# Kernel tuning notes

Hardware: AMD Instinct MI355X
Metric: run time of the kernel (lower is better)

The kernel has to match this reference:

```python
import jax, jax.numpy as jnp
import numpy as np

N_NODES = 50000


def gcn_conv(x, edge_index, W, b, n):
    # PyG GCNConv: xW, add self-loops, symmetric degree normalization,
    # scatter-add messages from source (row) to target (col).
    xw = x @ W
    row, col = edge_index[0], edge_index[1]
    loops = jnp.arange(n, dtype=edge_index.dtype)
    row = jnp.concatenate([row, loops])
    col = jnp.concatenate([col, loops])
    deg = jax.ops.segment_sum(jnp.ones(row.shape[0], dtype=xw.dtype), col, num_segments=n)
    dinv = jnp.where(deg > 0, jax.lax.rsqrt(deg), 0.0)
    norm = dinv[row] * dinv[col]  # [E+N]
    out = jax.ops.segment_sum(xw[row] * norm[:, None], col, num_segments=n)
    return out + b


def setup_inputs() -> dict:
    key = jax.random.key(0)
    ks = jax.random.split(key, 5)
    n, d_in, d_h, d_out, n_edges = N_NODES, 128, 128, 4, 600000
    x = jax.random.normal(ks[0], (n, d_in), dtype=jnp.float32)
    edge_index = jax.random.randint(ks[1], (2, n_edges), 0, n, dtype=jnp.int64)
    W1 = jax.random.normal(ks[2], (d_in, d_h), dtype=jnp.float32) * (1.0 / np.sqrt(d_in))
    b1 = jnp.zeros((d_h,), dtype=jnp.float32)
    W2 = jax.random.normal(ks[3], (d_h, d_h), dtype=jnp.float32) * (1.0 / np.sqrt(d_h))
    b2 = jnp.zeros((d_h,), dtype=jnp.float32)
    Wfc = jax.random.normal(ks[4], (2 * d_h, d_out), dtype=jnp.float32) * (1.0 / np.sqrt(2 * d_h))
    bfc = jnp.zeros((d_out,), dtype=jnp.float32)
    return {"x": x, "edge_index": edge_index, "W1": W1, "b1": b1,
            "W2": W2, "b2": b2, "Wfc": Wfc, "bfc": bfc}


def reference(x, edge_index, W1, b1, W2, b2, Wfc, bfc):
    n = x.shape[0]
    # dropout is identity at inference (training=False)
    h = jax.nn.relu(gcn_conv(x, edge_index, W1, b1, n))
    h = jax.nn.relu(gcn_conv(h, edge_index, W2, b2, n))
    # edge-level gather + concat + linear classifier
    edge_x = jnp.concatenate([h[edge_index[0]], h[edge_index[1]]], axis=-1)  # [E, 2*d_h]
    edge_scores = edge_x @ Wfc + bfc  # [E, d_out]
    return jax.nn.log_softmax(edge_scores, axis=1)
```

## Files before the change

kernel.cpp:

```cpp
#include <hip/hip_runtime.h>
#include <math.h>
#include <stdint.h>

#define D 128
#define SCAN_CHUNK 2048
#define LDA 136

typedef __attribute__((ext_vector_type(8))) short v8s;
typedef __attribute__((ext_vector_type(4))) float v4f;

static __device__ __forceinline__ uint16_t f2bf(float f) {
    uint32_t u = __float_as_uint(f);
    u = (u + 0x7fff + ((u >> 16) & 1)) >> 16;
    return (uint16_t)u;
}
static __device__ __forceinline__ float bf2f(uint16_t h) { return __uint_as_float((uint32_t)h << 16); }
static __device__ __forceinline__ float bf_lo(uint32_t u) { return __uint_as_float(u << 16); }
static __device__ __forceinline__ float bf_hi(uint32_t u) { return __uint_as_float(u & 0xffff0000u); }


__global__ void countpack_kernel(const int* __restrict__ col, int* __restrict__ cnt,
                                 int* __restrict__ rnk, int E,
                                 const float* __restrict__ W1, const float* __restrict__ W2,
                                 uint16_t* __restrict__ Wh, uint16_t* __restrict__ Wl) {
    int tid = blockIdx.x * blockDim.x + threadIdx.x;
    if (tid < 2 * 16384) {
        int layer = tid >> 14;
        int li = tid & 16383;
        int j = li & 7, lane = (li >> 3) & 63, f = li >> 9;
        int kstep = f >> 3, tile = f & 7;
        int k = kstep * 32 + ((lane >> 4) * 8) + j;
        int nn = tile * 16 + (lane & 15);
        const float* W = layer ? W2 : W1;
        float v = W[k * 128 + nn];
        uint16_t h = f2bf(v);
        Wh[tid] = h;
        Wl[tid] = f2bf(v - bf2f(h));
    }
    if (tid < E) rnk[tid] = atomicAdd(&cnt[col[tid]], 1);
}


__global__ __launch_bounds__(256) void scanA_kernel(const int* __restrict__ cnt,
                                                    int* __restrict__ bsum,
                                                    float* __restrict__ dinv, int n) {
    __shared__ int wsum[4];
    int b = blockIdx.x, t = threadIdx.x;
    int base = b * SCAN_CHUNK;
    int s = 0;
#pragma unroll
    for (int k = 0; k < SCAN_CHUNK / 256; k++) {
        int i = base + k * 256 + t;
        if (i < n) {
            int c = cnt[i];
            s += c;
            dinv[i] = rsqrtf((float)c + 1.0f);
        }
    }
#pragma unroll
    for (int off = 32; off > 0; off >>= 1) s += __shfl_xor(s, off, 64);
    if ((t & 63) == 0) wsum[t >> 6] = s;
    __syncthreads();
    if (t == 0) bsum[b] = wsum[0] + wsum[1] + wsum[2] + wsum[3];
}


__global__ __launch_bounds__(256) void scanC_kernel(const int* __restrict__ cnt,
                                                    const int* __restrict__ bsum,
                                                    int* __restrict__ offs, int n, int nb) {
    __shared__ int stage[SCAN_CHUNK];
    __shared__ int res[SCAN_CHUNK];
    __shared__ int tsum[256];
    __shared__ int sb[64];
    int b = blockIdx.x, t = threadIdx.x;
    if (t < 64) {
        int v = (t < nb) ? bsum[t] : 0;
        int inc = v;
#pragma unroll
        for (int off = 1; off < 64; off <<= 1) {
            int u = __shfl_up(inc, off, 64);
            if (t >= off) inc += u;
        }
        sb[t] = inc;
    }
    int base = b * SCAN_CHUNK;
#pragma unroll
    for (int k = 0; k < SCAN_CHUNK / 256; k++) {
        int i = base + k * 256 + t;
        stage[k * 256 + t] = (i < n) ? cnt[i] : 0;
    }
    __syncthreads();
    int my = 0;
#pragma unroll
    for (int j = 0; j < 8; j++) my += stage[t * 8 + j];
    tsum[t] = my;
    __syncthreads();
    for (int off = 1; off < 256; off <<= 1) {
        int v = (t >= off) ? tsum[t - off] : 0;
        __syncthreads();
        tsum[t] += v;
        __syncthreads();
    }
    int bbase = (b == 0) ? 0 : sb[b - 1];
    int run = tsum[t] - my + bbase;
#pragma unroll
    for (int j = 0; j < 8; j++) {
        res[t * 8 + j] = run;
        run += stage[t * 8 + j];
    }
    __syncthreads();
#pragma unroll
    for (int k = 0; k < SCAN_CHUNK / 256; k++) {
        int i = base + k * 256 + t;
        if (i < n) offs[i] = res[k * 256 + t];
    }
    if (b == gridDim.x - 1 && t == 0) offs[n] = sb[nb - 1];
}


static __device__ __forceinline__ void gemm_body(const uint16_t Ah[][LDA],
                                                 const uint16_t Al[][LDA],
                                                 const uint16_t* __restrict__ Wph,
                                                 const uint16_t* __restrict__ Wpl,
                                                 const float* __restrict__ dinv,
                                                 uint16_t* __restrict__ Cb,
                                                 int base_row, int M, int t) {
    int lane = t & 63, w = t >> 6;
    int m_l = lane & 15, quad = lane >> 4;
    int arow = w * 16 + m_l;

    v4f acc[8];
#pragma unroll
    for (int i = 0; i < 8; i++) acc[i] = (v4f){0.f, 0.f, 0.f, 0.f};

#pragma unroll
    for (int ks = 0; ks < 4; ks++) {
        v8s ah = *(const v8s*)&Ah[arow][ks * 32 + quad * 8];
        v8s al = *(const v8s*)&Al[arow][ks * 32 + quad * 8];
#pragma unroll
        for (int ti = 0; ti < 8; ti++) {
            int f = ks * 8 + ti;
            v8s bh = *(const v8s*)(Wph + ((size_t)(f * 64 + lane)) * 8);
            v8s bl = *(const v8s*)(Wpl + ((size_t)(f * 64 + lane)) * 8);
            acc[ti] = __builtin_amdgcn_mfma_f32_16x16x32_bf16(al, bh, acc[ti], 0, 0, 0);
            acc[ti] = __builtin_amdgcn_mfma_f32_16x16x32_bf16(ah, bl, acc[ti], 0, 0, 0);
            acc[ti] = __builtin_amdgcn_mfma_f32_16x16x32_bf16(ah, bh, acc[ti], 0, 0, 0);
        }
    }

    int rbase = base_row + w * 16 + quad * 4;
#pragma unroll
    for (int reg = 0; reg < 4; reg++) {
        int gr = rbase + reg;
        if (gr < M) {
            float di = dinv[gr];
#pragma unroll
            for (int ti = 0; ti < 8; ti++) {
                Cb[(size_t)gr * D + ti * 16 + m_l] = f2bf(di * acc[ti][reg]);
            }
        }
    }
}


__global__ __launch_bounds__(256) void fillgemm_kernel(const int* __restrict__ row,
                                                       const int* __restrict__ col,
                                                       const int* __restrict__ rnk,
                                                       const int* __restrict__ offs,
                                                       int* __restrict__ adj, int E,
                                                       const float* __restrict__ A,
                                                       const uint16_t* __restrict__ Wph,
                                                       const uint16_t* __restrict__ Wpl,
                                                       const float* __restrict__ dinv,
                                                       uint16_t* __restrict__ Cb, int M,
                                                       int nbG) {
    __shared__ uint16_t Ah[64][LDA];
    __shared__ uint16_t Al[64][LDA];
    int t = threadIdx.x;

    if (blockIdx.x >= nbG) {
        int e = (blockIdx.x - nbG) * 256 + t;
        if (e < E) adj[offs[col[e]] + rnk[e]] = row[e];
        return;
    }

    int base_row = blockIdx.x * 64;
#pragma unroll
    for (int kk = 0; kk < 8; kk++) {
        int idx = kk * 256 + t;
        int r = idx >> 5;
        int c4 = idx & 31;
        int gr = base_row + r;
        float4 f = (gr < M) ? *(const float4*)(A + (size_t)gr * D + c4 * 4)
                            : make_float4(0.f, 0.f, 0.f, 0.f);
        uint16_t h0 = f2bf(f.x), h1 = f2bf(f.y), h2 = f2bf(f.z), h3 = f2bf(f.w);
        uint16_t l0 = f2bf(f.x - bf2f(h0)), l1 = f2bf(f.y - bf2f(h1));
        uint16_t l2 = f2bf(f.z - bf2f(h2)), l3 = f2bf(f.w - bf2f(h3));
        *(ushort4*)&Ah[r][c4 * 4] = make_ushort4(h0, h1, h2, h3);
        *(ushort4*)&Al[r][c4 * 4] = make_ushort4(l0, l1, l2, l3);
    }
    __syncthreads();
    gemm_body(Ah, Al, Wph, Wpl, dinv, Cb, base_row, M, t);
}


__global__ __launch_bounds__(256) void agggemm_kernel(const uint32_t* __restrict__ xwb,
                                                      const int* __restrict__ adj,
                                                      const int* __restrict__ offs,
                                                      const float* __restrict__ dinv,
                                                      const float* __restrict__ bias,
                                                      const uint16_t* __restrict__ Wph,
                                                      const uint16_t* __restrict__ Wpl,
                                                      uint16_t* __restrict__ Cb, int M) {
    __shared__ uint16_t Ah[64][LDA];
    __shared__ uint16_t Al[64][LDA];
    int t = threadIdx.x, lane = t & 63, w = t >> 6;
    int base_row = blockIdx.x * 64;
    float2 bv = ((const float2*)bias)[lane];

    for (int rr = 0; rr < 8; rr++) {
        int rA = w * 16 + rr, rB = rA + 8;
        int iA = base_row + rA, iB = base_row + rB;
        float a0 = 0.f, a1 = 0.f, c0 = 0.f, c1 = 0.f;
        int jA = 0, eA = 0, jB = 0, eB = 0;
        if (iA < M) {
            uint32_t su = xwb[(size_t)iA * (D / 2) + lane];
            a0 = bf_lo(su); a1 = bf_hi(su);
            jA = offs[iA]; eA = offs[iA + 1];
        }
        if (iB < M) {
            uint32_t su = xwb[(size_t)iB * (D / 2) + lane];
            c0 = bf_lo(su); c1 = bf_hi(su);
            jB = offs[iB]; eB = offs[iB + 1];
        }
        while (jA + 7 < eA && jB + 7 < eB) {
            int xx[8], yy[8];
#pragma unroll
            for (int q = 0; q < 8; q++) { xx[q] = adj[jA + q]; yy[q] = adj[jB + q]; }
            uint32_t uA[8], uB[8];
#pragma unroll
            for (int q = 0; q < 8; q++) {
                uA[q] = xwb[(size_t)xx[q] * (D / 2) + lane];
                uB[q] = xwb[(size_t)yy[q] * (D / 2) + lane];
            }
#pragma unroll
            for (int q = 0; q < 8; q++) {
                a0 += bf_lo(uA[q]); a1 += bf_hi(uA[q]);
                c0 += bf_lo(uB[q]); c1 += bf_hi(uB[q]);
            }
            jA += 8; jB += 8;
        }
        for (; jA + 7 < eA; jA += 8) {
            int xx[8]; uint32_t uA[8];
#pragma unroll
            for (int q = 0; q < 8; q++) xx[q] = adj[jA + q];
#pragma unroll
            for (int q = 0; q < 8; q++) uA[q] = xwb[(size_t)xx[q] * (D / 2) + lane];
#pragma unroll
            for (int q = 0; q < 8; q++) { a0 += bf_lo(uA[q]); a1 += bf_hi(uA[q]); }
        }
        for (; jA + 3 < eA; jA += 4) {
            int x0 = adj[jA], x1 = adj[jA + 1], x2 = adj[jA + 2], x3 = adj[jA + 3];
            uint32_t u0 = xwb[(size_t)x0 * (D / 2) + lane];
            uint32_t u1 = xwb[(size_t)x1 * (D / 2) + lane];
            uint32_t u2 = xwb[(size_t)x2 * (D / 2) + lane];
            uint32_t u3 = xwb[(size_t)x3 * (D / 2) + lane];
            a0 += bf_lo(u0); a1 += bf_hi(u0);
            a0 += bf_lo(u1); a1 += bf_hi(u1);
            a0 += bf_lo(u2); a1 += bf_hi(u2);
            a0 += bf_lo(u3); a1 += bf_hi(u3);
        }
        for (; jA < eA; jA++) {
            uint32_t u = xwb[(size_t)adj[jA] * (D / 2) + lane];
            a0 += bf_lo(u); a1 += bf_hi(u);
        }
        for (; jB + 7 < eB; jB += 8) {
            int yy[8]; uint32_t uB[8];
#pragma unroll
            for (int q = 0; q < 8; q++) yy[q] = adj[jB + q];
#pragma unroll
            for (int q = 0; q < 8; q++) uB[q] = xwb[(size_t)yy[q] * (D / 2) + lane];
#pragma unroll
            for (int q = 0; q < 8; q++) { c0 += bf_lo(uB[q]); c1 += bf_hi(uB[q]); }
        }
        for (; jB + 3 < eB; jB += 4) {
            int y0 = adj[jB], y1 = adj[jB + 1], y2 = adj[jB + 2], y3 = adj[jB + 3];
            uint32_t u0 = xwb[(size_t)y0 * (D / 2) + lane];
            uint32_t u1 = xwb[(size_t)y1 * (D / 2) + lane];
            uint32_t u2 = xwb[(size_t)y2 * (D / 2) + lane];
            uint32_t u3 = xwb[(size_t)y3 * (D / 2) + lane];
            c0 += bf_lo(u0); c1 += bf_hi(u0);
            c0 += bf_lo(u1); c1 += bf_hi(u1);
            c0 += bf_lo(u2); c1 += bf_hi(u2);
            c0 += bf_lo(u3); c1 += bf_hi(u3);
        }
        for (; jB < eB; jB++) {
            uint32_t u = xwb[(size_t)adj[jB] * (D / 2) + lane];
            c0 += bf_lo(u); c1 += bf_hi(u);
        }
        float diA = (iA < M) ? dinv[iA] : 0.f;
        float diB = (iB < M) ? dinv[iB] : 0.f;
        float oA0 = fmaxf(fmaf(diA, a0, bv.x), 0.f);
        float oA1 = fmaxf(fmaf(diA, a1, bv.y), 0.f);
        float oB0 = fmaxf(fmaf(diB, c0, bv.x), 0.f);
        float oB1 = fmaxf(fmaf(diB, c1, bv.y), 0.f);
        if (iA >= M) { oA0 = 0.f; oA1 = 0.f; }
        if (iB >= M) { oB0 = 0.f; oB1 = 0.f; }
        uint16_t hA0 = f2bf(oA0), hA1 = f2bf(oA1);
        uint16_t lA0 = f2bf(oA0 - bf2f(hA0)), lA1 = f2bf(oA1 - bf2f(hA1));
        uint16_t hB0 = f2bf(oB0), hB1 = f2bf(oB1);
        uint16_t lB0 = f2bf(oB0 - bf2f(hB0)), lB1 = f2bf(oB1 - bf2f(hB1));
        *(ushort2*)&Ah[rA][2 * lane] = make_ushort2(hA0, hA1);
        *(ushort2*)&Al[rA][2 * lane] = make_ushort2(lA0, lA1);
        *(ushort2*)&Ah[rB][2 * lane] = make_ushort2(hB0, hB1);
        *(ushort2*)&Al[rB][2 * lane] = make_ushort2(lB0, lB1);
    }
    __syncthreads();
    gemm_body(Ah, Al, Wph, Wpl, dinv, Cb, base_row, M, t);
}


__global__ __launch_bounds__(256) void agg2pq_kernel(const uint32_t* __restrict__ xwb,
                                                     const int* __restrict__ adj,
                                                     const int* __restrict__ offs,
                                                     const float* __restrict__ dinv,
                                                     const float* __restrict__ bias,
                                                     const float* __restrict__ Wfc,
                                                     const float* __restrict__ bfc,
                                                     float* __restrict__ P1,
                                                     float* __restrict__ P2, int n) {
    int wave = (int)((blockIdx.x * (size_t)blockDim.x + threadIdx.x) >> 6);
    int lane = threadIdx.x & 63;
    if (wave >= n) return;
    int i = wave;
    uint32_t su = xwb[(size_t)i * (D / 2) + lane];
    float acc0 = bf_lo(su);
    float acc1 = bf_hi(su);
    int s = offs[i], e = offs[i + 1];
    int j = s;
    for (; j + 7 < e; j += 8) {
        int r0 = adj[j],     r1 = adj[j + 1], r2 = adj[j + 2], r3 = adj[j + 3];
        int r4 = adj[j + 4], r5 = adj[j + 5], r6 = adj[j + 6], r7 = adj[j + 7];
        uint32_t u0 = xwb[(size_t)r0 * (D / 2) + lane];
        uint32_t u1 = xwb[(size_t)r1 * (D / 2) + lane];
        uint32_t u2 = xwb[(size_t)r2 * (D / 2) + lane];
        uint32_t u3 = xwb[(size_t)r3 * (D / 2) + lane];
        uint32_t u4 = xwb[(size_t)r4 * (D / 2) + lane];
        uint32_t u5 = xwb[(size_t)r5 * (D / 2) + lane];
        uint32_t u6 = xwb[(size_t)r6 * (D / 2) + lane];
        uint32_t u7 = xwb[(size_t)r7 * (D / 2) + lane];
        acc0 += bf_lo(u0); acc1 += bf_hi(u0);
        acc0 += bf_lo(u1); acc1 += bf_hi(u1);
        acc0 += bf_lo(u2); acc1 += bf_hi(u2);
        acc0 += bf_lo(u3); acc1 += bf_hi(u3);
        acc0 += bf_lo(u4); acc1 += bf_hi(u4);
        acc0 += bf_lo(u5); acc1 += bf_hi(u5);
        acc0 += bf_lo(u6); acc1 += bf_hi(u6);
        acc0 += bf_lo(u7); acc1 += bf_hi(u7);
    }
    for (; j + 3 < e; j += 4) {
        int r0 = adj[j], r1 = adj[j + 1], r2 = adj[j + 2], r3 = adj[j + 3];
        uint32_t u0 = xwb[(size_t)r0 * (D / 2) + lane];
        uint32_t u1 = xwb[(size_t)r1 * (D / 2) + lane];
        uint32_t u2 = xwb[(size_t)r2 * (D / 2) + lane];
        uint32_t u3 = xwb[(size_t)r3 * (D / 2) + lane];
        acc0 += bf_lo(u0); acc1 += bf_hi(u0);
        acc0 += bf_lo(u1); acc1 += bf_hi(u1);
        acc0 += bf_lo(u2); acc1 += bf_hi(u2);
        acc0 += bf_lo(u3); acc1 += bf_hi(u3);
    }
    for (; j < e; j++) {
        int r = adj[j];
        uint32_t u = xwb[(size_t)r * (D / 2) + lane];
        acc0 += bf_lo(u); acc1 += bf_hi(u);
    }
    float di = dinv[i];
    float2 bv = ((const float2*)bias)[lane];
    float o0 = fmaxf(fmaf(di, acc0, bv.x), 0.f);
    float o1 = fmaxf(fmaf(di, acc1, bv.y), 0.f);

    const float4* W4 = (const float4*)Wfc;
    float4 wa = W4[2 * lane];
    float4 wb = W4[2 * lane + 1];
    float4 wc = W4[128 + 2 * lane];
    float4 wd = W4[129 + 2 * lane];
    float p0 = fmaf(o0, wa.x, o1 * wb.x), p1 = fmaf(o0, wa.y, o1 * wb.y);
    float p2 = fmaf(o0, wa.z, o1 * wb.z), p3 = fmaf(o0, wa.w, o1 * wb.w);
    float q0 = fmaf(o0, wc.x, o1 * wd.x), q1 = fmaf(o0, wc.y, o1 * wd.y);
    float q2 = fmaf(o0, wc.z, o1 * wd.z), q3 = fmaf(o0, wc.w, o1 * wd.w);
#pragma unroll
    for (int off = 1; off < 64; off <<= 1) {
        p0 += __shfl_xor(p0, off, 64);
        p1 += __shfl_xor(p1, off, 64);
        p2 += __shfl_xor(p2, off, 64);
        p3 += __shfl_xor(p3, off, 64);
        q0 += __shfl_xor(q0, off, 64);
        q1 += __shfl_xor(q1, off, 64);
        q2 += __shfl_xor(q2, off, 64);
        q3 += __shfl_xor(q3, off, 64);
    }
    if (lane == 0) {
        float4 bb = *(const float4*)bfc;
        *(float4*)(P1 + (size_t)i * 4) = make_float4(p0 + bb.x, p1 + bb.y, p2 + bb.z, p3 + bb.w);
        *(float4*)(P2 + (size_t)i * 4) = make_float4(q0, q1, q2, q3);
    }
}


__global__ __launch_bounds__(256) void edge2_kernel(const int* __restrict__ row,
                                                    const int* __restrict__ col,
                                                    const float* __restrict__ P1,
                                                    const float* __restrict__ P2,
                                                    float* __restrict__ out, int E) {
    int e = blockIdx.x * blockDim.x + threadIdx.x;
    if (e >= E) return;
    int r = row[e], c = col[e];
    float4 a = ((const float4*)P1)[r];
    float4 b = ((const float4*)P2)[c];
    float sx = a.x + b.x, sy = a.y + b.y, sz = a.z + b.z, sw = a.w + b.w;
    float m = fmaxf(fmaxf(sx, sy), fmaxf(sz, sw));
    float e0 = expf(sx - m), e1 = expf(sy - m), e2 = expf(sz - m), e3 = expf(sw - m);
    float lse = m + logf(e0 + e1 + e2 + e3);
    *(float4*)(out + (size_t)e * 4) = make_float4(sx - lse, sy - lse, sz - lse, sw - lse);
}


extern "C" void kernel_launch(void* const* d_in, const int* in_sizes, int n_in,
                              void* d_out, int out_size, void* d_ws, size_t ws_size,
                              hipStream_t stream) {
    const float* x   = (const float*)d_in[0];
    const int*   ei  = (const int*)d_in[1];
    const float* W1  = (const float*)d_in[2];
    const float* b1  = (const float*)d_in[3];
    const float* W2  = (const float*)d_in[4];
    const float* b2  = (const float*)d_in[5];
    const float* Wfc = (const float*)d_in[6];
    const float* bfc = (const float*)d_in[7];
    float* out = (float*)d_out;

    int n = in_sizes[0] / D;
    int E = in_sizes[1] / 2;
    const int* row = ei;
    const int* col = ei + E;

    int nbScan = (n + SCAN_CHUNK - 1) / SCAN_CHUNK;

    uint16_t* xwb  = (uint16_t*)d_ws;
    uint16_t* xwb2 = xwb + (size_t)n * D;
    int*      cnt  = (int*)(xwb2 + (size_t)n * D);
    int*      offs = cnt + n;
    int*      bsum = offs + (n + 4);
    int*      adj  = bsum + 64;
    int*      rnk  = adj + E;
    float*    dinv = (float*)(rnk + E);
    uint16_t* Wph  = (uint16_t*)(dinv + n);
    uint16_t* Wpl  = Wph + 2 * 16384;
    float*    P1   = (float*)(Wpl + 2 * 16384);
    float*    P2   = P1 + (size_t)n * 4;

    int nb_e = (E + 255) / 256;
    int nbG  = (n + 63) / 64;

    hipMemsetAsync(cnt, 0, (size_t)n * sizeof(int), stream);
    countpack_kernel<<<nb_e, 256, 0, stream>>>(col, cnt, rnk, E, W1, W2, Wph, Wpl);
    scanA_kernel<<<nbScan, 256, 0, stream>>>(cnt, bsum, dinv, n);
    scanC_kernel<<<nbScan, 256, 0, stream>>>(cnt, bsum, offs, n, nbScan);

    fillgemm_kernel<<<nbG + nb_e, 256, 0, stream>>>(row, col, rnk, offs, adj, E,
                                                    x, Wph, Wpl, dinv, xwb, n, nbG);

    agggemm_kernel<<<nbG, 256, 0, stream>>>((const uint32_t*)xwb, adj, offs, dinv, b1,
                                            Wph + 16384, Wpl + 16384, xwb2, n);

    agg2pq_kernel<<<(n + 3) / 4, 256, 0, stream>>>((const uint32_t*)xwb2, adj, offs, dinv, b2,
                                                   Wfc, bfc, P1, P2, n);

    edge2_kernel<<<nb_e, 256, 0, stream>>>(row, col, P1, P2, out, E);
}
```

Baseline: 235.7 us.

## Split fused aggregate+GEMM into separate agg1 and GEMM kernels; two nodes per wave

The fused layer-1 aggregation plus GEMM kernel is split in two. A standalone agg1 kernel writes the fp32 hidden activations to global memory, and a plain GEMM kernel reads them back through a shared staging helper. agg2pq now handles two nodes per wave, interleaving their gathers and sharing the weight loads. This trades an extra fp32 round trip through global memory (about 25 MB) and one more launch for finer-grained, better-balanced aggregation parallelism in place of 64-row blocks tied to the GEMM tile.

```diff
diff --git a/kernel.cpp b/kernel.cpp
--- a/kernel.cpp
+++ b/kernel.cpp
@@ -162,6 +162,25 @@
     }
 }
 
+static __device__ __forceinline__ void stage_tile(uint16_t Ah[][LDA], uint16_t Al[][LDA],
+                                                  const float* __restrict__ A,
+                                                  int base_row, int M, int t) {
+#pragma unroll
+    for (int kk = 0; kk < 8; kk++) {
+        int idx = kk * 256 + t;
+        int r = idx >> 5;
+        int c4 = idx & 31;
+        int gr = base_row + r;
+        float4 f = (gr < M) ? *(const float4*)(A + (size_t)gr * D + c4 * 4)
+                            : make_float4(0.f, 0.f, 0.f, 0.f);
+        uint16_t h0 = f2bf(f.x), h1 = f2bf(f.y), h2 = f2bf(f.z), h3 = f2bf(f.w);
+        uint16_t l0 = f2bf(f.x - bf2f(h0)), l1 = f2bf(f.y - bf2f(h1));
+        uint16_t l2 = f2bf(f.z - bf2f(h2)), l3 = f2bf(f.w - bf2f(h3));
+        *(ushort4*)&Ah[r][c4 * 4] = make_ushort4(h0, h1, h2, h3);
+        *(ushort4*)&Al[r][c4 * 4] = make_ushort4(l0, l1, l2, l3);
+    }
+}
+
 
 __global__ __launch_bounds__(256) void fillgemm_kernel(const int* __restrict__ row,
                                                        const int* __restrict__ col,
@@ -185,138 +204,127 @@
     }
 
     int base_row = blockIdx.x * 64;
-#pragma unroll
-    for (int kk = 0; kk < 8; kk++) {
-        int idx = kk * 256 + t;
-        int r = idx >> 5;
-        int c4 = idx & 31;
-        int gr = base_row + r;
-        float4 f = (gr < M) ? *(const float4*)(A + (size_t)gr * D + c4 * 4)
-                            : make_float4(0.f, 0.f, 0.f, 0.f);
-        uint16_t h0 = f2bf(f.x), h1 = f2bf(f.y), h2 = f2bf(f.z), h3 = f2bf(f.w);
-        uint16_t l0 = f2bf(f.x - bf2f(h0)), l1 = f2bf(f.y - bf2f(h1));
-        uint16_t l2 = f2bf(f.z - bf2f(h2)), l3 = f2bf(f.w - bf2f(h3));
-        *(ushort4*)&Ah[r][c4 * 4] = make_ushort4(h0, h1, h2, h3);
-        *(ushort4*)&Al[r][c4 * 4] = make_ushort4(l0, l1, l2, l3);
-    }
+    stage_tile(Ah, Al, A, base_row, M, t);
     __syncthreads();
     gemm_body(Ah, Al, Wph, Wpl, dinv, Cb, base_row, M, t);
 }
 
 
-__global__ __launch_bounds__(256) void agggemm_kernel(const uint32_t* __restrict__ xwb,
-                                                      const int* __restrict__ adj,
-                                                      const int* __restrict__ offs,
-                                                      const float* __restrict__ dinv,
-                                                      const float* __restrict__ bias,
-                                                      const uint16_t* __restrict__ Wph,
-                                                      const uint16_t* __restrict__ Wpl,
-                                                      uint16_t* __restrict__ Cb, int M) {
+__global__ __launch_bounds__(256) void gemm_kernel(const float* __restrict__ A,
+                                                   const uint16_t* __restrict__ Wph,
+                                                   const uint16_t* __restrict__ Wpl,
+                                                   const float* __restrict__ dinv,
+                                                   uint16_t* __restrict__ Cb, int M) {
     __shared__ uint16_t Ah[64][LDA];
     __shared__ uint16_t Al[64][LDA];
-    int t = threadIdx.x, lane = t & 63, w = t >> 6;
+    int t = threadIdx.x;
     int base_row = blockIdx.x * 64;
-    float2 bv = ((const float2*)bias)[lane];
-
-    for (int rr = 0; rr < 8; rr++) {
-        int rA = w * 16 + rr, rB = rA + 8;
-        int iA = base_row + rA, iB = base_row + rB;
-        float a0 = 0.f, a1 = 0.f, c0 = 0.f, c1 = 0.f;
-        int jA = 0, eA = 0, jB = 0, eB = 0;
-        if (iA < M) {
-            uint32_t su = xwb[(size_t)iA * (D / 2) + lane];
-            a0 = bf_lo(su); a1 = bf_hi(su);
-            jA = offs[iA]; eA = offs[iA + 1];
-        }
-        if (iB < M) {
-            uint32_t su = xwb[(size_t)iB * (D / 2) + lane];
-            c0 = bf_lo(su); c1 = bf_hi(su);
-            jB = offs[iB]; eB = offs[iB + 1];
-        }
-        while (jA + 7 < eA && jB + 7 < eB) {
-            int xx[8], yy[8];
-#pragma unroll
-            for (int q = 0; q < 8; q++) { xx[q] = adj[jA + q]; yy[q] = adj[jB + q]; }
-            uint32_t uA[8], uB[8];
-#pragma unroll
-            for (int q = 0; q < 8; q++) {
-                uA[q] = xwb[(size_t)xx[q] * (D / 2) + lane];
-                uB[q] = xwb[(size_t)yy[q] * (D / 2) + lane];
-            }
-#pragma unroll
-            for (int q = 0; q < 8; q++) {
-                a0 += bf_lo(uA[q]); a1 += bf_hi(uA[q]);
-                c0 += bf_lo(uB[q]); c1 += bf_hi(uB[q]);
-            }
-            jA += 8; jB += 8;
-        }
-        for (; jA + 7 < eA; jA += 8) {
-            int xx[8]; uint32_t uA[8];
-#pragma unroll
-            for (int q = 0; q < 8; q++) xx[q] = adj[jA + q];
-#pragma unroll
-            for (int q = 0; q < 8; q++) uA[q] = xwb[(size_t)xx[q] * (D / 2) + lane];
-#pragma unroll
-            for (int q = 0; q < 8; q++) { a0 += bf_lo(uA[q]); a1 += bf_hi(uA[q]); }
-        }
-        for (; jA + 3 < eA; jA += 4) {
-            int x0 = adj[jA], x1 = adj[jA + 1], x2 = adj[jA + 2], x3 = adj[jA + 3];
-            uint32_t u0 = xwb[(size_t)x0 * (D / 2) + lane];
-            uint32_t u1 = xwb[(size_t)x1 * (D / 2) + lane];
-            uint32_t u2 = xwb[(size_t)x2 * (D / 2) + lane];
-            uint32_t u3 = xwb[(size_t)x3 * (D / 2) + lane];
-            a0 += bf_lo(u0); a1 += bf_hi(u0);
-            a0 += bf_lo(u1); a1 += bf_hi(u1);
-            a0 += bf_lo(u2); a1 += bf_hi(u2);
-            a0 += bf_lo(u3); a1 += bf_hi(u3);
-        }
-        for (; jA < eA; jA++) {
-            uint32_t u = xwb[(size_t)adj[jA] * (D / 2) + lane];
-            a0 += bf_lo(u); a1 += bf_hi(u);
-        }
-        for (; jB + 7 < eB; jB += 8) {
-            int yy[8]; uint32_t uB[8];
-#pragma unroll
-            for (int q = 0; q < 8; q++) yy[q] = adj[jB + q];
-#pragma unroll
-            for (int q = 0; q < 8; q++) uB[q] = xwb[(size_t)yy[q] * (D / 2) + lane];
-#pragma unroll
-            for (int q = 0; q < 8; q++) { c0 += bf_lo(uB[q]); c1 += bf_hi(uB[q]); }
-        }
-        for (; jB + 3 < eB; jB += 4) {
-            int y0 = adj[jB], y1 = adj[jB + 1], y2 = adj[jB + 2], y3 = adj[jB + 3];
-            uint32_t u0 = xwb[(size_t)y0 * (D / 2) + lane];
-            uint32_t u1 = xwb[(size_t)y1 * (D / 2) + lane];
-            uint32_t u2 = xwb[(size_t)y2 * (D / 2) + lane];
-            uint32_t u3 = xwb[(size_t)y3 * (D / 2) + lane];
-            c0 += bf_lo(u0); c1 += bf_hi(u0);
-            c0 += bf_lo(u1); c1 += bf_hi(u1);
-            c0 += bf_lo(u2); c1 += bf_hi(u2);
-            c0 += bf_lo(u3); c1 += bf_hi(u3);
-        }
-        for (; jB < eB; jB++) {
-            uint32_t u = xwb[(size_t)adj[jB] * (D / 2) + lane];
-            c0 += bf_lo(u); c1 += bf_hi(u);
-        }
-        float diA = (iA < M) ? dinv[iA] : 0.f;
-        float diB = (iB < M) ? dinv[iB] : 0.f;
-        float oA0 = fmaxf(fmaf(diA, a0, bv.x), 0.f);
-        float oA1 = fmaxf(fmaf(diA, a1, bv.y), 0.f);
-        float oB0 = fmaxf(fmaf(diB, c0, bv.x), 0.f);
-        float oB1 = fmaxf(fmaf(diB, c1, bv.y), 0.f);
-        if (iA >= M) { oA0 = 0.f; oA1 = 0.f; }
-        if (iB >= M) { oB0 = 0.f; oB1 = 0.f; }
-        uint16_t hA0 = f2bf(oA0), hA1 = f2bf(oA1);
-        uint16_t lA0 = f2bf(oA0 - bf2f(hA0)), lA1 = f2bf(oA1 - bf2f(hA1));
-        uint16_t hB0 = f2bf(oB0), hB1 = f2bf(oB1);
-        uint16_t lB0 = f2bf(oB0 - bf2f(hB0)), lB1 = f2bf(oB1 - bf2f(hB1));
-        *(ushort2*)&Ah[rA][2 * lane] = make_ushort2(hA0, hA1);
-        *(ushort2*)&Al[rA][2 * lane] = make_ushort2(lA0, lA1);
-        *(ushort2*)&Ah[rB][2 * lane] = make_ushort2(hB0, hB1);
-        *(ushort2*)&Al[rB][2 * lane] = make_ushort2(lB0, lB1);
-    }
+    stage_tile(Ah, Al, A, base_row, M, t);
     __syncthreads();
     gemm_body(Ah, Al, Wph, Wpl, dinv, Cb, base_row, M, t);
+}
+
+
+__global__ __launch_bounds__(256) void agg1_kernel(const uint32_t* __restrict__ xwb,
+                                                   const int* __restrict__ adj,
+                                                   const int* __restrict__ offs,
+                                                   const float* __restrict__ dinv,
+                                                   const float* __restrict__ bias,
+                                                   float* __restrict__ hout, int n) {
+    int wave = (int)((blockIdx.x * (size_t)blockDim.x + threadIdx.x) >> 6);
+    int lane = threadIdx.x & 63;
+    int i0 = wave * 2, i1 = wave * 2 + 1;
+    if (i0 >= n) return;
+    bool has1 = (i1 < n);
+
+    float a0, a1, c0 = 0.f, c1 = 0.f;
+    uint32_t su0 = xwb[(size_t)i0 * (D / 2) + lane];
+    a0 = bf_lo(su0); a1 = bf_hi(su0);
+    int jA = offs[i0], eA = offs[i0 + 1];
+    int jB = 0, eB = 0;
+    if (has1) {
+        uint32_t su1 = xwb[(size_t)i1 * (D / 2) + lane];
+        c0 = bf_lo(su1); c1 = bf_hi(su1);
+        jB = offs[i1]; eB = offs[i1 + 1];
+    }
+
+    while (jA + 7 < eA && jB + 7 < eB) {
+        int xx[8], yy[8];
+#pragma unroll
+        for (int q = 0; q < 8; q++) { xx[q] = adj[jA + q]; yy[q] = adj[jB + q]; }
+        uint32_t uA[8], uB[8];
+#pragma unroll
+        for (int q = 0; q < 8; q++) {
+            uA[q] = xwb[(size_t)xx[q] * (D / 2) + lane];
+            uB[q] = xwb[(size_t)yy[q] * (D / 2) + lane];
+        }
+#pragma unroll
+        for (int q = 0; q < 8; q++) {
+            a0 += bf_lo(uA[q]); a1 += bf_hi(uA[q]);
+            c0 += bf_lo(uB[q]); c1 += bf_hi(uB[q]);
+        }
+        jA += 8; jB += 8;
+    }
+    for (; jA + 7 < eA; jA += 8) {
+        int xx[8]; uint32_t uA[8];
+#pragma unroll
+        for (int q = 0; q < 8; q++) xx[q] = adj[jA + q];
+#pragma unroll
+        for (int q = 0; q < 8; q++) uA[q] = xwb[(size_t)xx[q] * (D / 2) + lane];
+#pragma unroll
+        for (int q = 0; q < 8; q++) { a0 += bf_lo(uA[q]); a1 += bf_hi(uA[q]); }
+    }
+    for (; jA + 3 < eA; jA += 4) {
+        int x0 = adj[jA], x1 = adj[jA + 1], x2 = adj[jA + 2], x3 = adj[jA + 3];
+        uint32_t u0 = xwb[(size_t)x0 * (D / 2) + lane];
+        uint32_t u1 = xwb[(size_t)x1 * (D / 2) + lane];
+        uint32_t u2 = xwb[(size_t)x2 * (D / 2) + lane];
+        uint32_t u3 = xwb[(size_t)x3 * (D / 2) + lane];
+        a0 += bf_lo(u0); a1 += bf_hi(u0);
+        a0 += bf_lo(u1); a1 += bf_hi(u1);
+        a0 += bf_lo(u2); a1 += bf_hi(u2);
+        a0 += bf_lo(u3); a1 += bf_hi(u3);
+    }
+    for (; jA < eA; jA++) {
+        uint32_t u = xwb[(size_t)adj[jA] * (D / 2) + lane];
+        a0 += bf_lo(u); a1 += bf_hi(u);
+    }
+    for (; jB + 7 < eB; jB += 8) {
+        int yy[8]; uint32_t uB[8];
+#pragma unroll
+        for (int q = 0; q < 8; q++) yy[q] = adj[jB + q];
+#pragma unroll
+        for (int q = 0; q < 8; q++) uB[q] = xwb[(size_t)yy[q] * (D / 2) + lane];
+#pragma unroll
+        for (int q = 0; q < 8; q++) { c0 += bf_lo(uB[q]); c1 += bf_hi(uB[q]); }
+    }
+    for (; jB + 3 < eB; jB += 4) {
+        int y0 = adj[jB], y1 = adj[jB + 1], y2 = adj[jB + 2], y3 = adj[jB + 3];
+        uint32_t u0 = xwb[(size_t)y0 * (D / 2) + lane];
+        uint32_t u1 = xwb[(size_t)y1 * (D / 2) + lane];
+        uint32_t u2 = xwb[(size_t)y2 * (D / 2) + lane];
+        uint32_t u3 = xwb[(size_t)y3 * (D / 2) + lane];
+        c0 += bf_lo(u0); c1 += bf_hi(u0);
+        c0 += bf_lo(u1); c1 += bf_hi(u1);
+        c0 += bf_lo(u2); c1 += bf_hi(u2);
+        c0 += bf_lo(u3); c1 += bf_hi(u3);
+    }
+    for (; jB < eB; jB++) {
+        uint32_t u = xwb[(size_t)adj[jB] * (D / 2) + lane];
+        c0 += bf_lo(u); c1 += bf_hi(u);
+    }
+
+    float2 bv = ((const float2*)bias)[lane];
+    float di0 = dinv[i0];
+    float o0 = fmaxf(fmaf(di0, a0, bv.x), 0.f);
+    float o1 = fmaxf(fmaf(di0, a1, bv.y), 0.f);
+    ((float2*)(hout + (size_t)i0 * D))[lane] = make_float2(o0, o1);
+    if (has1) {
+        float di1 = dinv[i1];
+        float o2 = fmaxf(fmaf(di1, c0, bv.x), 0.f);
+        float o3 = fmaxf(fmaf(di1, c1, bv.y), 0.f);
+        ((float2*)(hout + (size_t)i1 * D))[lane] = make_float2(o2, o3);
+    }
 }
 
 
@@ -331,53 +339,95 @@
                                                      float* __restrict__ P2, int n) {
     int wave = (int)((blockIdx.x * (size_t)blockDim.x + threadIdx.x) >> 6);
     int lane = threadIdx.x & 63;
-    if (wave >= n) return;
-    int i = wave;
-    uint32_t su = xwb[(size_t)i * (D / 2) + lane];
-    float acc0 = bf_lo(su);
-    float acc1 = bf_hi(su);
-    int s = offs[i], e = offs[i + 1];
-    int j = s;
-    for (; j + 7 < e; j += 8) {
-        int r0 = adj[j],     r1 = adj[j + 1], r2 = adj[j + 2], r3 = adj[j + 3];
-        int r4 = adj[j + 4], r5 = adj[j + 5], r6 = adj[j + 6], r7 = adj[j + 7];
-        uint32_t u0 = xwb[(size_t)r0 * (D / 2) + lane];
-        uint32_t u1 = xwb[(size_t)r1 * (D / 2) + lane];
-        uint32_t u2 = xwb[(size_t)r2 * (D / 2) + lane];
-        uint32_t u3 = xwb[(size_t)r3 * (D / 2) + lane];
-        uint32_t u4 = xwb[(size_t)r4 * (D / 2) + lane];
-        uint32_t u5 = xwb[(size_t)r5 * (D / 2) + lane];
-        uint32_t u6 = xwb[(size_t)r6 * (D / 2) + lane];
-        uint32_t u7 = xwb[(size_t)r7 * (D / 2) + lane];
-        acc0 += bf_lo(u0); acc1 += bf_hi(u0);
-        acc0 += bf_lo(u1); acc1 += bf_hi(u1);
-        acc0 += bf_lo(u2); acc1 += bf_hi(u2);
-        acc0 += bf_lo(u3); acc1 += bf_hi(u3);
-        acc0 += bf_lo(u4); acc1 += bf_hi(u4);
-        acc0 += bf_lo(u5); acc1 += bf_hi(u5);
-        acc0 += bf_lo(u6); acc1 += bf_hi(u6);
-        acc0 += bf_lo(u7); acc1 += bf_hi(u7);
-    }
-    for (; j + 3 < e; j += 4) {
-        int r0 = adj[j], r1 = adj[j + 1], r2 = adj[j + 2], r3 = adj[j + 3];
-        uint32_t u0 = xwb[(size_t)r0 * (D / 2) + lane];
-        uint32_t u1 = xwb[(size_t)r1 * (D / 2) + lane];
-        uint32_t u2 = xwb[(size_t)r2 * (D / 2) + lane];
-        uint32_t u3 = xwb[(size_t)r3 * (D / 2) + lane];
-        acc0 += bf_lo(u0); acc1 += bf_hi(u0);
-        acc0 += bf_lo(u1); acc1 += bf_hi(u1);
-        acc0 += bf_lo(u2); acc1 += bf_hi(u2);
-        acc0 += bf_lo(u3); acc1 += bf_hi(u3);
-    }
-    for (; j < e; j++) {
-        int r = adj[j];
-        uint32_t u = xwb[(size_t)r * (D / 2) + lane];
-        acc0 += bf_lo(u); acc1 += bf_hi(u);
-    }
-    float di = dinv[i];
+    int i0 = wave * 2, i1 = wave * 2 + 1;
+    if (i0 >= n) return;
+    bool has1 = (i1 < n);
+
+    float a0, a1, c0 = 0.f, c1 = 0.f;
+    uint32_t su0 = xwb[(size_t)i0 * (D / 2) + lane];
+    a0 = bf_lo(su0); a1 = bf_hi(su0);
+    int jA = offs[i0], eA = offs[i0 + 1];
+    int jB = 0, eB = 0;
+    if (has1) {
+        uint32_t su1 = xwb[(size_t)i1 * (D / 2) + lane];
+        c0 = bf_lo(su1); c1 = bf_hi(su1);
+        jB = offs[i1]; eB = offs[i1 + 1];
+    }
+
+    while (jA + 7 < eA && jB + 7 < eB) {
+        int xx[8], yy[8];
+#pragma unroll
+        for (int q = 0; q < 8; q++) { xx[q] = adj[jA + q]; yy[q] = adj[jB + q]; }
+        uint32_t uA[8], uB[8];
+#pragma unroll
+        for (int q = 0; q < 8; q++) {
+            uA[q] = xwb[(size_t)xx[q] * (D / 2) + lane];
+            uB[q] = xwb[(size_t)yy[q] * (D / 2) + lane];
+        }
+#pragma unroll
+        for (int q = 0; q < 8; q++) {
+            a0 += bf_lo(uA[q]); a1 += bf_hi(uA[q]);
+            c0 += bf_lo(uB[q]); c1 += bf_hi(uB[q]);
+        }
+        jA += 8; jB += 8;
+    }
+    for (; jA + 7 < eA; jA += 8) {
+        int xx[8]; uint32_t uA[8];
+#pragma unroll
+        for (int q = 0; q < 8; q++) xx[q] = adj[jA + q];
+#pragma unroll
+        for (int q = 0; q < 8; q++) uA[q] = xwb[(size_t)xx[q] * (D / 2) + lane];
+#pragma unroll
+        for (int q = 0; q < 8; q++) { a0 += bf_lo(uA[q]); a1 += bf_hi(uA[q]); }
+    }
+    for (; jA + 3 < eA; jA += 4) {
+        int x0 = adj[jA], x1 = adj[jA + 1], x2 = adj[jA + 2], x3 = adj[jA + 3];
+        uint32_t u0 = xwb[(size_t)x0 * (D / 2) + lane];
+        uint32_t u1 = xwb[(size_t)x1 * (D / 2) + lane];
+        uint32_t u2 = xwb[(size_t)x2 * (D / 2) + lane];
+        uint32_t u3 = xwb[(size_t)x3 * (D / 2) + lane];
+        a0 += bf_lo(u0); a1 += bf_hi(u0);
+        a0 += bf_lo(u1); a1 += bf_hi(u1);
+        a0 += bf_lo(u2); a1 += bf_hi(u2);
+        a0 += bf_lo(u3); a1 += bf_hi(u3);
+    }
+    for (; jA < eA; jA++) {
+        uint32_t u = xwb[(size_t)adj[jA] * (D / 2) + lane];
+        a0 += bf_lo(u); a1 += bf_hi(u);
+    }
+    for (; jB + 7 < eB; jB += 8) {
+        int yy[8]; uint32_t uB[8];
+#pragma unroll
+        for (int q = 0; q < 8; q++) yy[q] = adj[jB + q];
+#pragma unroll
+        for (int q = 0; q < 8; q++) uB[q] = xwb[(size_t)yy[q] * (D / 2) + lane];
+#pragma unroll
+        for (int q = 0; q < 8; q++) { c0 += bf_lo(uB[q]); c1 += bf_hi(uB[q]); }
+    }
+    for (; jB + 3 < eB; jB += 4) {
+        int y0 = adj[jB], y1 = adj[jB + 1], y2 = adj[jB + 2], y3 = adj[jB + 3];
+        uint32_t u0 = xwb[(size_t)y0 * (D / 2) + lane];
+        uint32_t u1 = xwb[(size_t)y1 * (D / 2) + lane];
+        uint32_t u2 = xwb[(size_t)y2 * (D / 2) + lane];
+        uint32_t u3 = xwb[(size_t)y3 * (D / 2) + lane];
+        c0 += bf_lo(u0); c1 += bf_hi(u0);
+        c0 += bf_lo(u1); c1 += bf_hi(u1);
+        c0 += bf_lo(u2); c1 += bf_hi(u2);
+        c0 += bf_lo(u3); c1 += bf_hi(u3);
+    }
+    for (; jB < eB; jB++) {
+        uint32_t u = xwb[(size_t)adj[jB] * (D / 2) + lane];
+        c0 += bf_lo(u); c1 += bf_hi(u);
+    }
+
     float2 bv = ((const float2*)bias)[lane];
-    float o0 = fmaxf(fmaf(di, acc0, bv.x), 0.f);
-    float o1 = fmaxf(fmaf(di, acc1, bv.y), 0.f);
+    float di0 = dinv[i0];
+    float o0 = fmaxf(fmaf(di0, a0, bv.x), 0.f);
+    float o1 = fmaxf(fmaf(di0, a1, bv.y), 0.f);
+    float di1 = has1 ? dinv[i1] : 0.f;
+    float o2 = fmaxf(fmaf(di1, c0, bv.x), 0.f);
+    float o3 = fmaxf(fmaf(di1, c1, bv.y), 0.f);
+    if (!has1) { o2 = 0.f; o3 = 0.f; }
 
     const float4* W4 = (const float4*)Wfc;
     float4 wa = W4[2 * lane];
@@ -388,6 +438,10 @@
     float p2 = fmaf(o0, wa.z, o1 * wb.z), p3 = fmaf(o0, wa.w, o1 * wb.w);
     float q0 = fmaf(o0, wc.x, o1 * wd.x), q1 = fmaf(o0, wc.y, o1 * wd.y);
     float q2 = fmaf(o0, wc.z, o1 * wd.z), q3 = fmaf(o0, wc.w, o1 * wd.w);
+    float r0 = fmaf(o2, wa.x, o3 * wb.x), r1 = fmaf(o2, wa.y, o3 * wb.y);
+    float r2 = fmaf(o2, wa.z, o3 * wb.z), r3 = fmaf(o2, wa.w, o3 * wb.w);
+    float s0 = fmaf(o2, wc.x, o3 * wd.x), s1 = fmaf(o2, wc.y, o3 * wd.y);
+    float s2 = fmaf(o2, wc.z, o3 * wd.z), s3 = fmaf(o2, wc.w, o3 * wd.w);
 #pragma unroll
     for (int off = 1; off < 64; off <<= 1) {
         p0 += __shfl_xor(p0, off, 64);
@@ -398,11 +452,23 @@
         q1 += __shfl_xor(q1, off, 64);
         q2 += __shfl_xor(q2, off, 64);
         q3 += __shfl_xor(q3, off, 64);
+        r0 += __shfl_xor(r0, off, 64);
+        r1 += __shfl_xor(r1, off, 64);
+        r2 += __shfl_xor(r2, off, 64);
+        r3 += __shfl_xor(r3, off, 64);
+        s0 += __shfl_xor(s0, off, 64);
+        s1 += __shfl_xor(s1, off, 64);
+        s2 += __shfl_xor(s2, off, 64);
+        s3 += __shfl_xor(s3, off, 64);
     }
     if (lane == 0) {
         float4 bb = *(const float4*)bfc;
-        *(float4*)(P1 + (size_t)i * 4) = make_float4(p0 + bb.x, p1 + bb.y, p2 + bb.z, p3 + bb.w);
-        *(float4*)(P2 + (size_t)i * 4) = make_float4(q0, q1, q2, q3);
+        *(float4*)(P1 + (size_t)i0 * 4) = make_float4(p0 + bb.x, p1 + bb.y, p2 + bb.z, p3 + bb.w);
+        *(float4*)(P2 + (size_t)i0 * 4) = make_float4(q0, q1, q2, q3);
+        if (has1) {
+            *(float4*)(P1 + (size_t)i1 * 4) = make_float4(r0 + bb.x, r1 + bb.y, r2 + bb.z, r3 + bb.w);
+            *(float4*)(P2 + (size_t)i1 * 4) = make_float4(s0, s1, s2, s3);
+        }
     }
 }
 
@@ -447,7 +513,8 @@
 
     uint16_t* xwb  = (uint16_t*)d_ws;
     uint16_t* xwb2 = xwb + (size_t)n * D;
-    int*      cnt  = (int*)(xwb2 + (size_t)n * D);
+    float*    h    = (float*)(xwb2 + (size_t)n * D);
+    int*      cnt  = (int*)(h + (size_t)n * D);
     int*      offs = cnt + n;
     int*      bsum = offs + (n + 4);
     int*      adj  = bsum + 64;
@@ -460,6 +527,8 @@
 
     int nb_e = (E + 255) / 256;
     int nbG  = (n + 63) / 64;
+    int nWaves = (n + 1) / 2;
+    int nbA  = (nWaves + 3) / 4;
 
     hipMemsetAsync(cnt, 0, (size_t)n * sizeof(int), stream);
     countpack_kernel<<<nb_e, 256, 0, stream>>>(col, cnt, rnk, E, W1, W2, Wph, Wpl);
@@ -469,11 +538,12 @@
     fillgemm_kernel<<<nbG + nb_e, 256, 0, stream>>>(row, col, rnk, offs, adj, E,
                                                     x, Wph, Wpl, dinv, xwb, n, nbG);
 
-    agggemm_kernel<<<nbG, 256, 0, stream>>>((const uint32_t*)xwb, adj, offs, dinv, b1,
-                                            Wph + 16384, Wpl + 16384, xwb2, n);
-
-    agg2pq_kernel<<<(n + 3) / 4, 256, 0, stream>>>((const uint32_t*)xwb2, adj, offs, dinv, b2,
-                                                   Wfc, bfc, P1, P2, n);
+    agg1_kernel<<<nbA, 256, 0, stream>>>((const uint32_t*)xwb, adj, offs, dinv, b1, h, n);
+
+    gemm_kernel<<<nbG, 256, 0, stream>>>(h, Wph + 16384, Wpl + 16384, dinv, xwb2, n);
+
+    agg2pq_kernel<<<nbA, 256, 0, stream>>>((const uint32_t*)xwb2, adj, offs, dinv, b2,
+                                           Wfc, bfc, P1, P2, n);
 
     edge2_kernel<<<nb_e, 256, 0, stream>>>(row, col, P1, P2, out, E);
 }
```

Result: no change. 232.0 us, median of 2 (-1.5%).
